# Kernel optimization log

Hardware: AMD Instinct MI355X
Metric: run time of the kernel (lower is better)

Reference implementation:

```python
import jax, jax.numpy as jnp
import numpy as np

# 7 axial hex directions (dy, dx) including center, matching HexConv2d.DIRS
DIRS = [(0, 0), (1, 0), (0, 1), (-1, 1), (-1, 0), (0, -1), (1, -1)]


def _shift(x, dy, dx):
    """torch.roll-style shift with zero fill at wrapped edges. x: [B,C,H,W]."""
    sx, sy = -dx, -dy
    y = jnp.roll(x, shift=(sy, sx), axis=(2, 3))
    if sy > 0:
        y = y.at[:, :, :sy, :].set(0)
    elif sy < 0:
        y = y.at[:, :, sy:, :].set(0)
    if sx > 0:
        y = y.at[:, :, :, :sx].set(0)
    elif sx < 0:
        y = y.at[:, :, :, sx:].set(0)
    return y


def _hex_mask(H, dtype):
    size = H // 2
    q = jnp.arange(-size, size + 1)
    Q, R = jnp.meshgrid(q, q, indexing='ij')
    S = -Q - R
    # |Q|<=size and |R|<=size hold by construction; only |S|<=size cuts corners
    mask = ((jnp.abs(Q) <= size) & (jnp.abs(R) <= size) & (jnp.abs(S) <= size))
    return mask.astype(dtype)[None, None]  # [1,1,H,W]


def setup_inputs() -> dict:
    key = jax.random.key(0)
    k1, k2, k3 = jax.random.split(key, 3)
    B, Cin, Cout, H = 32, 256, 256, 49
    x = jax.random.normal(k1, (B, Cin, H, H), dtype=jnp.float32)
    weight = jax.random.normal(k2, (Cout, Cin, 7), dtype=jnp.float32) * 0.02
    bias = jax.random.normal(k3, (Cout,), dtype=jnp.float32) * 0.02
    return {"x": x, "weight": weight, "bias": bias}


def reference(x, weight, bias):
    mask = _hex_mask(x.shape[2], x.dtype)          # [1,1,H,W]
    x = x * mask
    # [7,B,C,H,W]: shifted+masked neighbor maps
    nbr = jnp.stack([_shift(x, dy, dx) for (dy, dx) in DIRS], axis=0) * mask
    # fused 1x1 conv over (channel, direction): weight [O,C,7]
    y = jnp.einsum('nbchw,ocn->bohw', nbr, weight) + bias[None, :, None, None]
    return y * mask
```

## Files before the change

### kernel.cpp

```cpp
#include <hip/hip_runtime.h>


typedef __attribute__((ext_vector_type(8))) short short8;
typedef __attribute__((ext_vector_type(4))) short short4v;
typedef __attribute__((ext_vector_type(4))) float floatx4;

#define NPIX   2401
#define W50    50
#define PREAL  2450
#define XBLEAD 56
#define XBROWS 2672
#define PT6    160
#define NT6    16
#define NSEG6  17
#define BUF6   (2*NSEG6*1024)
#define XB3_BYTES ((size_t)32*XBROWS*256*2)
#define WP_BYTES  917504ULL
#define WS_NEED3  (XB3_BYTES + WP_BYTES)
#define NPADROW 271

__device__ __forceinline__ unsigned short f2bf(float f) {
  unsigned u = __builtin_bit_cast(unsigned, f);
  u += 0x7fffu + ((u >> 16) & 1u);
  return (unsigned short)(u >> 16);
}

__global__ void prep_w_kernel(const float* __restrict__ w, unsigned short* __restrict__ wp) {
  int t = blockIdx.x * 256 + threadIdx.x;
  int l  = t & 63;
  int ot = (t >> 6) & 15;
  int kc = (t >> 10) & 7;
  int n  = t >> 13;
  int o  = ot * 16 + (l & 15);
  int cb = kc * 32 + ((l >> 4) * 8);
  const float* src = w + (size_t)(o * 256 + cb) * 7 + n;
  short8 pk;
#pragma unroll
  for (int j = 0; j < 8; ++j) pk[j] = (short)f2bf(src[j * 7]);
  ((short8*)wp)[t] = pk;
}

__global__ void zero_pads5(unsigned short* __restrict__ xb) {
  int idx = blockIdx.x * 256 + threadIdx.x;
  if (idx >= 32 * NPADROW * 32) return;
  int c16 = idx & 31;
  int rr  = idx >> 5;
  int pr  = rr % NPADROW;
  int b   = rr / NPADROW;
  int row;
  if (pr < 56)        row = pr;
  else if (pr < 105)  row = 105 + 50 * (pr - 56);
  else                row = 2506 + (pr - 105);
  short8 z = {0,0,0,0,0,0,0,0};
  *(short8*)(xb + ((size_t)b * XBROWS + row) * 256 + c16 * 8) = z;
}

__global__ __launch_bounds__(256)
void prep_x4(const float* __restrict__ x, unsigned short* __restrict__ xb) {
  __shared__ unsigned short t[64][68];
  const int tid = threadIdx.x;
  const int span = blockIdx.x, cg = blockIdx.y, b = blockIdx.z;
  const int s0 = span * 64;
  {
    const int chl = tid >> 2, i4 = tid & 3;
    const float* src = x + ((size_t)(b * 256 + cg * 64 + chl)) * NPIX;
    const int rbase = s0 + i4 * 16;
#pragma unroll
    for (int it = 0; it < 4; ++it) {
      int r = rbase + it * 4;
      float vv[4] = {0.f, 0.f, 0.f, 0.f};
      if (r + 3 < NPIX) {
        float4 v = *(const float4*)(src + r);
        vv[0] = v.x; vv[1] = v.y; vv[2] = v.z; vv[3] = v.w;
      } else {
#pragma unroll
        for (int e = 0; e < 4; ++e) if (r + e < NPIX) vv[e] = src[r + e];
      }
      short4v u = {0, 0, 0, 0};
#pragma unroll
      for (int e = 0; e < 4; ++e) {
        int re = r + e;
        unsigned short uu = 0;
        if (re < NPIX) {
          int h = re / 49, w = re - h * 49, s = h + w;
          if (s >= 24 && s <= 72) uu = f2bf(vv[e]);
        }
        u[e] = (short)uu;
      }
      *(short4v*)&t[chl][i4 * 16 + it * 4] = u;
    }
  }
  __syncthreads();
  const int pp = tid >> 3;
  const int co = tid & 7;
  unsigned d[8];
#pragma unroll
  for (int k = 0; k < 8; ++k) d[k] = *(const unsigned*)&t[co * 8 + k][pp * 2];
  uint4 lo, hi;
  {
    unsigned l0[4], h0[4];
#pragma unroll
    for (int m = 0; m < 4; ++m) {
      unsigned a = d[2 * m], bq = d[2 * m + 1];
      l0[m] = (a & 0xffffu) | (bq << 16);
      h0[m] = (a >> 16) | (bq & 0xffff0000u);
    }
    lo = make_uint4(l0[0], l0[1], l0[2], l0[3]);
    hi = make_uint4(h0[0], h0[1], h0[2], h0[3]);
  }
  const int r_lo = s0 + pp * 2, r_hi = r_lo + 1;
  if (r_lo < NPIX) {
    int prow = r_lo + r_lo / 49 + XBLEAD;
    *(uint4*)(xb + ((size_t)b * XBROWS + prow) * 256 + cg * 64 + co * 8) = lo;
  }
  if (r_hi < NPIX) {
    int prow = r_hi + r_hi / 49 + XBLEAD;
    *(uint4*)(xb + ((size_t)b * XBROWS + prow) * 256 + cg * 64 + co * 8) = hi;
  }
}

__global__ __launch_bounds__(512, 2)
void hexconv_v10(const unsigned short* __restrict__ xb,
                 const unsigned short* __restrict__ wp,
                 const float* __restrict__ bias,
                 float* __restrict__ out) {
  __shared__ __attribute__((aligned(16))) unsigned char smem[2 * BUF6];

  const int tid  = threadIdx.x;
  const int lane = tid & 63;
  const int wv   = tid >> 6;
  const int col  = lane & 15;
  const int quad = lane >> 4;
  const int oh   = wv >> 1;
  const int ph   = wv & 1;

  const int pt = blockIdx.x;
  const int b  = blockIdx.y;
  const int P0 = pt * PT6;
  const int phase = ((pt + b) & 3) * 2;

  const int OFF[7] = {0, 50, 1, -49, -50, -1, 49};

  int ba[7];
#pragma unroll
  for (int n = 0; n < 7; ++n) {
    int r0 = col + 56 + OFF[n];
    int r64 = r0 << 6;
    ba[n] = (((r64 + quad * 16) ^ ((r64 >> 3) & 0x30))) + ph * 5120;
  }

  const int gpart = (lane & 3) ^ ((lane >> 3) & 3);
  const char* gsrc0 = (const char*)(xb + ((size_t)b * XBROWS + (size_t)P0) * 256)
                      + (lane >> 2) * 512 + gpart * 16;

  auto stage2 = [&](int buf, int kc0) {
    char* ldsb = (char*)smem + buf * BUF6;
    for (int u = wv; u < 2 * NSEG6; u += 8) {
      int kk = (u >= NSEG6) ? 1 : 0;
      int s  = u - kk * NSEG6;
      __builtin_amdgcn_global_load_lds(
          (const __attribute__((address_space(1))) unsigned int*)
              (gsrc0 + (size_t)s * 8192 + (kc0 + kk) * 64),
          (__attribute__((address_space(3))) unsigned int*)(ldsb + u * 1024), 16, 0, 0);
    }
  };

  const char* wbase = (const char*)wp + (size_t)(oh * 4) * 1024 + lane * 16;

  floatx4 acc[4][5];
#pragma unroll
  for (int ii = 0; ii < 4; ++ii)
#pragma unroll
    for (int j = 0; j < 5; ++j) acc[ii][j] = (floatx4){0.f, 0.f, 0.f, 0.f};

  stage2(0, phase);
  __syncthreads();

  for (int i = 0; i < 4; ++i) {
    const int kc0  = (2 * i + phase) & 7;
    const int kc0n = (2 * i + 2 + phase) & 7;
    if (i < 3) stage2((i + 1) & 1, kc0n);
    const char* bufp = (const char*)smem + (i & 1) * BUF6;
#pragma unroll
    for (int n = 0; n < 7; ++n) {
#pragma unroll
      for (int kk = 0; kk < 2; ++kk) {
        const int kc = kc0 + kk;
        short8 af[4];
#pragma unroll
        for (int ii = 0; ii < 4; ++ii)
          af[ii] = *(const short8*)(wbase + ((size_t)((n * 8 + kc) * 16 + ii)) * 1024);
        const char* bp = bufp + kk * (NSEG6 * 1024) + ba[n];
        short8 bfv[5];
#pragma unroll
        for (int j = 0; j < 5; ++j)
          bfv[j] = *(const short8*)(bp + j * 1024);
        __builtin_amdgcn_s_setprio(1);
#pragma unroll
        for (int j = 0; j < 5; ++j)
#pragma unroll
          for (int ii = 0; ii < 4; ++ii)
            acc[ii][j] = __builtin_amdgcn_mfma_f32_16x16x32_bf16(af[ii], bfv[j], acc[ii][j], 0, 0, 0);
        __builtin_amdgcn_s_setprio(0);
      }
    }
    if (i < 3) __syncthreads();
  }

  const int ob = oh * 64;
#pragma unroll
  for (int ii = 0; ii < 4; ++ii) {
    floatx4 bv = *(const floatx4*)(bias + ob + ii * 16 + quad * 4);
#pragma unroll
    for (int j = 0; j < 5; ++j)
#pragma unroll
      for (int rr = 0; rr < 4; ++rr) acc[ii][j][rr] += bv[rr];
  }

#pragma unroll
  for (int j = 0; j < 5; ++j) {
    int p = P0 + ph * 80 + j * 16 + col;
    int h = p / W50;
    int w = p - h * W50;
    if (w >= 49 || p >= PREAL) continue;
    bool m = (h + w >= 24) && (h + w <= 72);
    int ridx = h * 49 + w;
#pragma unroll
    for (int ii = 0; ii < 4; ++ii) {
      float* dst = out + ((b * 256 + ob + ii * 16 + quad * 4) * NPIX + ridx);
#pragma unroll
      for (int rr = 0; rr < 4; ++rr) {
        float v = m ? acc[ii][j][rr] : 0.f;
        dst[rr * NPIX] = v;
      }
    }
  }
}

#define PITCH  40
#define V1WIN  168
#define V1ZROW 168
__global__ __launch_bounds__(256)
void hexconv_v1(const float* __restrict__ x,
                const unsigned short* __restrict__ wp,
                const float* __restrict__ bias,
                float* __restrict__ out) {
  __shared__ unsigned short sm[(V1ZROW + 2) * PITCH];
  const int tid = threadIdx.x, lane = tid & 63, wv = tid >> 6;
  const int col = lane & 15, quad = lane >> 4;
  const int pt = blockIdx.x, b = blockIdx.y;
  const int P0 = pt * 64, win_start = P0 - 52;
  if (tid < PITCH * 2) sm[V1ZROW * PITCH + tid] = 0;
  const int OFF[7] = {0, 49, 1, -48, -49, -1, 48};
  const int DXP = (1 << 2) | (1 << 3), DXN = (1 << 5) | (1 << 6);
  int baddr[4][7];
#pragma unroll
  for (int j = 0; j < 4; ++j) {
    int pix = P0 + j * 16 + col;
    int wj = pix % 49;
    int rowbase = pix - win_start;
#pragma unroll
    for (int n = 0; n < 7; ++n) {
      bool bad = (((DXP >> n) & 1) && wj == 48) || (((DXN >> n) & 1) && wj == 0);
      int row = bad ? V1ZROW : (rowbase + OFF[n]);
      baddr[j][n] = row * (PITCH * 2) + quad * 16;
    }
  }
  int sp[3], sgp[3]; bool sok[3];
#pragma unroll
  for (int pi = 0; pi < 3; ++pi) {
    int p = lane + pi * 64, gp = win_start + p;
    sp[pi] = p; sgp[pi] = gp;
    bool hm = false;
    if (gp >= 0 && gp < NPIX) { int h = gp / 49, w = gp - h * 49, s = h + w; hm = (s >= 24 && s <= 72); }
    sok[pi] = (p < V1WIN) && hm;
  }
  floatx4 acc[4][4];
#pragma unroll
  for (int i = 0; i < 4; ++i)
#pragma unroll
    for (int j = 0; j < 4; ++j) acc[i][j] = (floatx4){0.f, 0.f, 0.f, 0.f};
  const short8* wpv = (const short8*)wp;
  const int wslot = wv * 4;
  for (int kc = 0; kc < 8; ++kc) {
    __syncthreads();
#pragma unroll
    for (int ci = 0; ci < 8; ++ci) {
      int c = ci * 4 + wv;
      const float* src = x + ((size_t)(b * 256 + kc * 32 + c)) * NPIX;
#pragma unroll
      for (int pi = 0; pi < 3; ++pi) {
        if (sp[pi] < V1WIN) {
          float v = sok[pi] ? src[sgp[pi]] : 0.f;
          sm[sp[pi] * PITCH + c] = f2bf(v);
        }
      }
    }
    __syncthreads();
#pragma unroll
    for (int n = 0; n < 7; ++n) {
      short8 af[4];
#pragma unroll
      for (int i = 0; i < 4; ++i)
        af[i] = wpv[((size_t)((n * 8 + kc) * 16 + wslot + i)) * 64 + lane];
      short8 bf[4];
#pragma unroll
      for (int j = 0; j < 4; ++j)
        bf[j] = *(const short8*)((const char*)sm + baddr[j][n]);
#pragma unroll
      for (int i = 0; i < 4; ++i)
#pragma unroll
        for (int j = 0; j < 4; ++j)
          acc[i][j] = __builtin_amdgcn_mfma_f32_16x16x32_bf16(af[i], bf[j], acc[i][j], 0, 0, 0);
    }
  }
  const int ob = wv * 64;
  floatx4 bv[4];
#pragma unroll
  for (int i = 0; i < 4; ++i)
    bv[i] = *(const floatx4*)(bias + ob + i * 16 + quad * 4);
#pragma unroll
  for (int j = 0; j < 4; ++j) {
    int pix = P0 + j * 16 + col;
    if (pix >= NPIX) continue;
    int h = pix / 49, w = pix - h * 49;
    bool m = (h + w >= 24 && h + w <= 72);
#pragma unroll
    for (int i = 0; i < 4; ++i) {
      int o = ob + i * 16 + quad * 4;
      float* dst = out + ((size_t)(b * 256 + o)) * NPIX + pix;
#pragma unroll
      for (int r = 0; r < 4; ++r) {
        float v = m ? (acc[i][j][r] + bv[i][r]) : 0.f;
        dst[(size_t)r * NPIX] = v;
      }
    }
  }
}

extern "C" void kernel_launch(void* const* d_in, const int* in_sizes, int n_in,
                              void* d_out, int out_size, void* d_ws, size_t ws_size,
                              hipStream_t stream) {
  const float* x    = (const float*)d_in[0];
  const float* w    = (const float*)d_in[1];
  const float* bias = (const float*)d_in[2];
  float* out = (float*)d_out;

  if (ws_size >= WS_NEED3) {
    unsigned short* xb = (unsigned short*)d_ws;
    unsigned short* wp = (unsigned short*)((char*)d_ws + XB3_BYTES);
    zero_pads5<<<(32 * NPADROW * 32 + 255) / 256, 256, 0, stream>>>(xb);
    prep_w_kernel<<<224, 256, 0, stream>>>(w, wp);
    prep_x4<<<dim3(38, 4, 32), 256, 0, stream>>>(x, xb);
    hexconv_v10<<<dim3(NT6, 32), 512, 0, stream>>>(xb, wp, bias, out);
  } else {
    unsigned short* wp = (unsigned short*)d_ws;
    prep_w_kernel<<<224, 256, 0, stream>>>(w, wp);
    hexconv_v1<<<dim3(38, 32), 256, 0, stream>>>(x, wp, bias, out);
  }
}
```

Before: 239.9 us.

## Merge prep kernels into one launch and shrink conv tiles to 80 pixels

The three preprocessing kernels (pad zeroing, weight packing, input transpose to bf16) become one launch that dispatches on block index. The main conv kernel now uses 256-thread blocks that each cover 80 pixels instead of 512 threads over 160. This halves the LDS staging buffer and doubles the grid to 32x32 blocks, with a swizzled pixel-tile order. The aim is to cut launch overhead and improve occupancy and load balance, at the cost of more redundant halo and weight fetches per pixel.

```diff
diff --git a/kernel.cpp b/kernel.cpp
--- a/kernel.cpp
+++ b/kernel.cpp
@@ -10,133 +10,148 @@
 #define PREAL  2450
 #define XBLEAD 56
 #define XBROWS 2672
-#define PT6    160
-#define NT6    16
-#define NSEG6  17
-#define BUF6   (2*NSEG6*1024)
+#define PT11   80
+#define NT11   32
+#define NSEG11 12
+#define KCOL11 (NSEG11*1024)
+#define BUF11  (2*KCOL11)
 #define XB3_BYTES ((size_t)32*XBROWS*256*2)
 #define WP_BYTES  917504ULL
 #define WS_NEED3  (XB3_BYTES + WP_BYTES)
 #define NPADROW 271
 
+#define X4_BLKS 4864
+#define Z_BLKS  1084
+#define W_BLKS  224
+#define PREP_BLKS (X4_BLKS + Z_BLKS + W_BLKS)
+
 __device__ __forceinline__ unsigned short f2bf(float f) {
   unsigned u = __builtin_bit_cast(unsigned, f);
   u += 0x7fffu + ((u >> 16) & 1u);
   return (unsigned short)(u >> 16);
 }
 
-__global__ void prep_w_kernel(const float* __restrict__ w, unsigned short* __restrict__ wp) {
-  int t = blockIdx.x * 256 + threadIdx.x;
-  int l  = t & 63;
-  int ot = (t >> 6) & 15;
-  int kc = (t >> 10) & 7;
-  int n  = t >> 13;
+__device__ __forceinline__ void prep_w_body(const float* __restrict__ w,
+                                            unsigned short* __restrict__ wp, int tt) {
+  int l  = tt & 63;
+  int ot = (tt >> 6) & 15;
+  int kc = (tt >> 10) & 7;
+  int n  = tt >> 13;
   int o  = ot * 16 + (l & 15);
   int cb = kc * 32 + ((l >> 4) * 8);
   const float* src = w + (size_t)(o * 256 + cb) * 7 + n;
   short8 pk;
 #pragma unroll
   for (int j = 0; j < 8; ++j) pk[j] = (short)f2bf(src[j * 7]);
-  ((short8*)wp)[t] = pk;
-}
-
-__global__ void zero_pads5(unsigned short* __restrict__ xb) {
-  int idx = blockIdx.x * 256 + threadIdx.x;
-  if (idx >= 32 * NPADROW * 32) return;
-  int c16 = idx & 31;
-  int rr  = idx >> 5;
-  int pr  = rr % NPADROW;
-  int b   = rr / NPADROW;
-  int row;
-  if (pr < 56)        row = pr;
-  else if (pr < 105)  row = 105 + 50 * (pr - 56);
-  else                row = 2506 + (pr - 105);
-  short8 z = {0,0,0,0,0,0,0,0};
-  *(short8*)(xb + ((size_t)b * XBROWS + row) * 256 + c16 * 8) = z;
+  ((short8*)wp)[tt] = pk;
 }
 
 __global__ __launch_bounds__(256)
-void prep_x4(const float* __restrict__ x, unsigned short* __restrict__ xb) {
+void prep_all(const float* __restrict__ x, const float* __restrict__ w,
+              unsigned short* __restrict__ xb, unsigned short* __restrict__ wp) {
   __shared__ unsigned short t[64][68];
   const int tid = threadIdx.x;
-  const int span = blockIdx.x, cg = blockIdx.y, b = blockIdx.z;
-  const int s0 = span * 64;
-  {
-    const int chl = tid >> 2, i4 = tid & 3;
-    const float* src = x + ((size_t)(b * 256 + cg * 64 + chl)) * NPIX;
-    const int rbase = s0 + i4 * 16;
-#pragma unroll
-    for (int it = 0; it < 4; ++it) {
-      int r = rbase + it * 4;
-      float vv[4] = {0.f, 0.f, 0.f, 0.f};
-      if (r + 3 < NPIX) {
-        float4 v = *(const float4*)(src + r);
-        vv[0] = v.x; vv[1] = v.y; vv[2] = v.z; vv[3] = v.w;
-      } else {
-#pragma unroll
-        for (int e = 0; e < 4; ++e) if (r + e < NPIX) vv[e] = src[r + e];
-      }
-      short4v u = {0, 0, 0, 0};
-#pragma unroll
-      for (int e = 0; e < 4; ++e) {
-        int re = r + e;
-        unsigned short uu = 0;
-        if (re < NPIX) {
-          int h = re / 49, w = re - h * 49, s = h + w;
-          if (s >= 24 && s <= 72) uu = f2bf(vv[e]);
+  const int blk = blockIdx.x;
+
+  if (blk < X4_BLKS) {
+    const int l = blk;
+    const int span = l % 38, cg = (l / 38) & 3, b = l / 152;
+    const int s0 = span * 64;
+    {
+      const int chl = tid >> 2, i4 = tid & 3;
+      const float* src = x + ((size_t)(b * 256 + cg * 64 + chl)) * NPIX;
+      const int rbase = s0 + i4 * 16;
+#pragma unroll
+      for (int it = 0; it < 4; ++it) {
+        int r = rbase + it * 4;
+        float vv[4] = {0.f, 0.f, 0.f, 0.f};
+        if (r + 3 < NPIX) {
+          float4 v = *(const float4*)(src + r);
+          vv[0] = v.x; vv[1] = v.y; vv[2] = v.z; vv[3] = v.w;
+        } else {
+#pragma unroll
+          for (int e = 0; e < 4; ++e) if (r + e < NPIX) vv[e] = src[r + e];
         }
-        u[e] = (short)uu;
-      }
-      *(short4v*)&t[chl][i4 * 16 + it * 4] = u;
-    }
-  }
-  __syncthreads();
-  const int pp = tid >> 3;
-  const int co = tid & 7;
-  unsigned d[8];
-#pragma unroll
-  for (int k = 0; k < 8; ++k) d[k] = *(const unsigned*)&t[co * 8 + k][pp * 2];
-  uint4 lo, hi;
-  {
-    unsigned l0[4], h0[4];
-#pragma unroll
-    for (int m = 0; m < 4; ++m) {
-      unsigned a = d[2 * m], bq = d[2 * m + 1];
-      l0[m] = (a & 0xffffu) | (bq << 16);
-      h0[m] = (a >> 16) | (bq & 0xffff0000u);
-    }
-    lo = make_uint4(l0[0], l0[1], l0[2], l0[3]);
-    hi = make_uint4(h0[0], h0[1], h0[2], h0[3]);
-  }
-  const int r_lo = s0 + pp * 2, r_hi = r_lo + 1;
-  if (r_lo < NPIX) {
-    int prow = r_lo + r_lo / 49 + XBLEAD;
-    *(uint4*)(xb + ((size_t)b * XBROWS + prow) * 256 + cg * 64 + co * 8) = lo;
-  }
-  if (r_hi < NPIX) {
-    int prow = r_hi + r_hi / 49 + XBLEAD;
-    *(uint4*)(xb + ((size_t)b * XBROWS + prow) * 256 + cg * 64 + co * 8) = hi;
-  }
-}
-
-__global__ __launch_bounds__(512, 2)
-void hexconv_v10(const unsigned short* __restrict__ xb,
+        short4v u = {0, 0, 0, 0};
+#pragma unroll
+        for (int e = 0; e < 4; ++e) {
+          int re = r + e;
+          unsigned short uu = 0;
+          if (re < NPIX) {
+            int h = re / 49, ww = re - h * 49, s = h + ww;
+            if (s >= 24 && s <= 72) uu = f2bf(vv[e]);
+          }
+          u[e] = (short)uu;
+        }
+        *(short4v*)&t[chl][i4 * 16 + it * 4] = u;
+      }
+    }
+    __syncthreads();
+    const int pp = tid >> 3;
+    const int co = tid & 7;
+    unsigned d[8];
+#pragma unroll
+    for (int k = 0; k < 8; ++k) d[k] = *(const unsigned*)&t[co * 8 + k][pp * 2];
+    uint4 lo, hi;
+    {
+      unsigned l0[4], h0[4];
+#pragma unroll
+      for (int m = 0; m < 4; ++m) {
+        unsigned a = d[2 * m], bq = d[2 * m + 1];
+        l0[m] = (a & 0xffffu) | (bq << 16);
+        h0[m] = (a >> 16) | (bq & 0xffff0000u);
+      }
+      lo = make_uint4(l0[0], l0[1], l0[2], l0[3]);
+      hi = make_uint4(h0[0], h0[1], h0[2], h0[3]);
+    }
+    const int r_lo = s0 + pp * 2, r_hi = r_lo + 1;
+    if (r_lo < NPIX) {
+      int prow = r_lo + r_lo / 49 + XBLEAD;
+      *(uint4*)(xb + ((size_t)b * XBROWS + prow) * 256 + cg * 64 + co * 8) = lo;
+    }
+    if (r_hi < NPIX) {
+      int prow = r_hi + r_hi / 49 + XBLEAD;
+      *(uint4*)(xb + ((size_t)b * XBROWS + prow) * 256 + cg * 64 + co * 8) = hi;
+    }
+  } else if (blk < X4_BLKS + Z_BLKS) {
+    int idx = (blk - X4_BLKS) * 256 + tid;
+    if (idx >= 32 * NPADROW * 32) return;
+    int c16 = idx & 31;
+    int rr  = idx >> 5;
+    int pr  = rr % NPADROW;
+    int b   = rr / NPADROW;
+    int row;
+    if (pr < 56)        row = pr;
+    else if (pr < 105)  row = 105 + 50 * (pr - 56);
+    else                row = 2506 + (pr - 105);
+    short8 z = {0,0,0,0,0,0,0,0};
+    *(short8*)(xb + ((size_t)b * XBROWS + row) * 256 + c16 * 8) = z;
+  } else {
+    prep_w_body(w, wp, (blk - X4_BLKS - Z_BLKS) * 256 + tid);
+  }
+}
+
+__global__ void prep_w_kernel(const float* __restrict__ w, unsigned short* __restrict__ wp) {
+  prep_w_body(w, wp, blockIdx.x * 256 + threadIdx.x);
+}
+
+__global__ __launch_bounds__(256, 3)
+void hexconv_v11(const unsigned short* __restrict__ xb,
                  const unsigned short* __restrict__ wp,
                  const float* __restrict__ bias,
                  float* __restrict__ out) {
-  __shared__ __attribute__((aligned(16))) unsigned char smem[2 * BUF6];
+  __shared__ __attribute__((aligned(16))) unsigned char smem[2 * BUF11];
 
   const int tid  = threadIdx.x;
   const int lane = tid & 63;
   const int wv   = tid >> 6;
   const int col  = lane & 15;
   const int quad = lane >> 4;
-  const int oh   = wv >> 1;
-  const int ph   = wv & 1;
-
-  const int pt = blockIdx.x;
+
+  const int bx = blockIdx.x;
+  const int pt = (bx & 7) * 4 + (bx >> 3);
   const int b  = blockIdx.y;
-  const int P0 = pt * PT6;
+  const int P0 = pt * PT11;
   const int phase = ((pt + b) & 3) * 2;
 
   const int OFF[7] = {0, 50, 1, -49, -50, -1, 49};
@@ -146,7 +161,7 @@
   for (int n = 0; n < 7; ++n) {
     int r0 = col + 56 + OFF[n];
     int r64 = r0 << 6;
-    ba[n] = (((r64 + quad * 16) ^ ((r64 >> 3) & 0x30))) + ph * 5120;
+    ba[n] = (r64 + quad * 16) ^ ((r64 >> 3) & 0x30);
   }
 
   const int gpart = (lane & 3) ^ ((lane >> 3) & 3);
@@ -154,10 +169,10 @@
                       + (lane >> 2) * 512 + gpart * 16;
 
   auto stage2 = [&](int buf, int kc0) {
-    char* ldsb = (char*)smem + buf * BUF6;
-    for (int u = wv; u < 2 * NSEG6; u += 8) {
-      int kk = (u >= NSEG6) ? 1 : 0;
-      int s  = u - kk * NSEG6;
+    char* ldsb = (char*)smem + buf * BUF11;
+    for (int u = wv; u < 2 * NSEG11; u += 4) {
+      int kk = (u >= NSEG11) ? 1 : 0;
+      int s  = u - kk * NSEG11;
       __builtin_amdgcn_global_load_lds(
           (const __attribute__((address_space(1))) unsigned int*)
               (gsrc0 + (size_t)s * 8192 + (kc0 + kk) * 64),
@@ -165,7 +180,7 @@
     }
   };
 
-  const char* wbase = (const char*)wp + (size_t)(oh * 4) * 1024 + lane * 16;
+  const char* wbase = (const char*)wp + (size_t)(wv * 4) * 1024 + lane * 16;
 
   floatx4 acc[4][5];
 #pragma unroll
@@ -180,7 +195,7 @@
     const int kc0  = (2 * i + phase) & 7;
     const int kc0n = (2 * i + 2 + phase) & 7;
     if (i < 3) stage2((i + 1) & 1, kc0n);
-    const char* bufp = (const char*)smem + (i & 1) * BUF6;
+    const char* bufp = (const char*)smem + (i & 1) * BUF11;
 #pragma unroll
     for (int n = 0; n < 7; ++n) {
 #pragma unroll
@@ -190,7 +205,7 @@
 #pragma unroll
         for (int ii = 0; ii < 4; ++ii)
           af[ii] = *(const short8*)(wbase + ((size_t)((n * 8 + kc) * 16 + ii)) * 1024);
-        const char* bp = bufp + kk * (NSEG6 * 1024) + ba[n];
+        const char* bp = bufp + kk * KCOL11 + ba[n];
         short8 bfv[5];
 #pragma unroll
         for (int j = 0; j < 5; ++j)
@@ -207,7 +222,7 @@
     if (i < 3) __syncthreads();
   }
 
-  const int ob = oh * 64;
+  const int ob = wv * 64;
 #pragma unroll
   for (int ii = 0; ii < 4; ++ii) {
     floatx4 bv = *(const floatx4*)(bias + ob + ii * 16 + quad * 4);
@@ -219,7 +234,7 @@
 
 #pragma unroll
   for (int j = 0; j < 5; ++j) {
-    int p = P0 + ph * 80 + j * 16 + col;
+    int p = P0 + j * 16 + col;
     int h = p / W50;
     int w = p - h * W50;
     if (w >= 49 || p >= PREAL) continue;
@@ -349,10 +364,8 @@
   if (ws_size >= WS_NEED3) {
     unsigned short* xb = (unsigned short*)d_ws;
     unsigned short* wp = (unsigned short*)((char*)d_ws + XB3_BYTES);
-    zero_pads5<<<(32 * NPADROW * 32 + 255) / 256, 256, 0, stream>>>(xb);
-    prep_w_kernel<<<224, 256, 0, stream>>>(w, wp);
-    prep_x4<<<dim3(38, 4, 32), 256, 0, stream>>>(x, xb);
-    hexconv_v10<<<dim3(NT6, 32), 512, 0, stream>>>(xb, wp, bias, out);
+    prep_all<<<PREP_BLKS, 256, 0, stream>>>(x, w, xb, wp);
+    hexconv_v11<<<dim3(NT11, 32), 256, 0, stream>>>(xb, wp, bias, out);
   } else {
     unsigned short* wp = (unsigned short*)d_ws;
     prep_w_kernel<<<224, 256, 0, stream>>>(w, wp);
```

Measured after the change: 233.2 us. 2.8% less time.
